# Performance work log

Hardware: AMD Instinct MI355X
Metric: run time of the kernel (lower is better)

## Reference

```python
import jax, jax.numpy as jnp
import numpy as np

E = 8          # num_experts
TOP_K = 2      # experts per token
D = 1024       # hidden_size
F = 2048       # intermediate_size
B, S = 2, 2048


def setup_inputs() -> dict:
    key = jax.random.key(0)
    k0, k1, k2, k3, k4 = jax.random.split(key, 5)
    return {
        "hidden_states": jax.random.normal(k0, (B, S, D), dtype=jnp.float32),
        "gate_w": jax.random.normal(k1, (D, E), dtype=jnp.float32) * 0.02,
        "w1": jax.random.normal(k2, (E, D, F), dtype=jnp.float32) * 0.02,
        "w2": jax.random.normal(k3, (E, F, D), dtype=jnp.float32) * 0.02,
        "w3": jax.random.normal(k4, (E, D, F), dtype=jnp.float32) * 0.02,
    }


def reference(hidden_states, gate_w, w1, w2, w3):
    b, s, d = hidden_states.shape
    x = hidden_states.reshape(-1, d)                       # [T, D]
    router_logits = x @ gate_w                             # [T, E]
    probs = jax.nn.softmax(router_logits, axis=-1)
    top_w, top_i = jax.lax.top_k(probs, TOP_K)             # [T, K]
    top_w = top_w / jnp.sum(top_w, axis=-1, keepdims=True)

    out = jnp.zeros_like(x)
    for e in range(E):
        # combine weight for expert e per token (0 if not routed here)
        w_e = jnp.sum(jnp.where(top_i == e, top_w, 0.0), axis=-1)   # [T]
        act = jax.nn.silu(x @ w1[e]) * (x @ w3[e])                  # [T, F]
        out = out + (act @ w2[e]) * w_e[:, None]
    return out.reshape(b, s, d)
```

## Files before the change

kernel.cpp:

```cpp
#include <hip/hip_runtime.h>

#define T_TOK 4096
#define D_DIM 1024
#define F_DIM 2048
#define E_NUM 8
#define MAX_TILES 136

typedef __attribute__((ext_vector_type(8))) short bf16x8;
typedef __attribute__((ext_vector_type(4))) float f32x4;

__device__ __forceinline__ unsigned short f2bf(float f) {
  unsigned u = __builtin_bit_cast(unsigned, f);
  unsigned r = 0x7FFFu + ((u >> 16) & 1u);
  return (unsigned short)((u + r) >> 16);
}

__device__ __forceinline__ void gload16(const unsigned short* g, unsigned short* l) {
  __builtin_amdgcn_global_load_lds(
      (const __attribute__((address_space(1))) unsigned int*)g,
      (__attribute__((address_space(3))) unsigned int*)l, 16, 0, 0);
}

__device__ __forceinline__ f32x4 mfma16(bf16x8 a, bf16x8 b, f32x4 c) {
  return __builtin_amdgcn_mfma_f32_16x16x32_bf16(a, b, c, 0, 0, 0);
}

__global__ __launch_bounds__(256) void transpose_all_kernel(
    const float* __restrict__ w1, const float* __restrict__ w3,
    const float* __restrict__ w2,
    unsigned short* __restrict__ W1t, unsigned short* __restrict__ W3t,
    unsigned short* __restrict__ W2t) {
  __shared__ float tile[64][65];
  int z = blockIdx.z;
  int which = z >> 3, e = z & 7;
  const float* src; unsigned short* dst; int M, N;
  if (which == 0)      { src = w1; dst = W1t; M = D_DIM; N = F_DIM; }
  else if (which == 1) { src = w3; dst = W3t; M = D_DIM; N = F_DIM; }
  else                 { src = w2; dst = W2t; M = F_DIM; N = D_DIM; }
  src += (size_t)e * M * N; dst += (size_t)e * M * N;
  int bid = blockIdx.y * gridDim.x + blockIdx.x;
  int nbx = N / 64;
  int i0 = (bid / nbx) * 64, j0 = (bid % nbx) * 64;
  int tid = threadIdx.x;
  int lr = tid >> 4;
  int lc = (tid & 15) * 4;
  #pragma unroll
  for (int p = 0; p < 4; p++) {
    int row = p * 16 + lr;
    float4 v = *(const float4*)&src[(size_t)(i0 + row) * N + j0 + lc];
    tile[row][lc + 0] = v.x; tile[row][lc + 1] = v.y;
    tile[row][lc + 2] = v.z; tile[row][lc + 3] = v.w;
  }
  __syncthreads();
  #pragma unroll
  for (int p = 0; p < 4; p++) {
    int orow = p * 16 + lr;
    unsigned short b0 = f2bf(tile[lc + 0][orow]);
    unsigned short b1 = f2bf(tile[lc + 1][orow]);
    unsigned short b2 = f2bf(tile[lc + 2][orow]);
    unsigned short b3 = f2bf(tile[lc + 3][orow]);
    uint2 o;
    o.x = b0 | ((unsigned)b1 << 16);
    o.y = b2 | ((unsigned)b3 << 16);
    *(uint2*)&dst[(size_t)(j0 + orow) * M + i0 + lc] = o;
  }
}

__global__ __launch_bounds__(256) void logits_kernel(const float* __restrict__ x,
                                                     const float* __restrict__ gw,
                                                     int* __restrict__ route_e,
                                                     float2* __restrict__ route_w,
                                                     unsigned short* __restrict__ Xb) {
  int lane = threadIdx.x & 63;
  int t = blockIdx.x * 4 + (threadIdx.x >> 6);
  float acc[E_NUM];
  #pragma unroll
  for (int e = 0; e < E_NUM; e++) acc[e] = 0.f;
  const float* xr = x + (size_t)t * D_DIM;
  unsigned short* xbr = Xb + (size_t)t * D_DIM;
  #pragma unroll
  for (int j = 0; j < D_DIM / 64; j++) {
    int d = lane + 64 * j;
    float xv = xr[d];
    xbr[d] = f2bf(xv);
    const float4* g = reinterpret_cast<const float4*>(gw + (size_t)d * E_NUM);
    float4 g0 = g[0], g1 = g[1];
    acc[0] += xv * g0.x; acc[1] += xv * g0.y; acc[2] += xv * g0.z; acc[3] += xv * g0.w;
    acc[4] += xv * g1.x; acc[5] += xv * g1.y; acc[6] += xv * g1.z; acc[7] += xv * g1.w;
  }
  #pragma unroll
  for (int e = 0; e < E_NUM; e++) {
    #pragma unroll
    for (int off = 32; off > 0; off >>= 1) acc[e] += __shfl_xor(acc[e], off);
  }
  if (lane == 0) {
    int e1 = 0; float l1 = acc[0];
    #pragma unroll
    for (int e = 1; e < E_NUM; e++) { if (acc[e] > l1) { l1 = acc[e]; e1 = e; } }
    int e2 = -1; float l2 = -1e30f;
    #pragma unroll
    for (int e = 0; e < E_NUM; e++) { if (e != e1 && acc[e] > l2) { l2 = acc[e]; e2 = e; } }
    float wa = 1.f / (1.f + expf(l2 - l1));
    float wb = 1.f / (1.f + expf(l1 - l2));
    route_e[t] = e1 | (e2 << 8);
    route_w[t] = make_float2(wa, wb);
  }
}

__global__ __launch_bounds__(1024) void scatter_kernel(
    const int* __restrict__ route_e, const float2* __restrict__ route_w,
    int* __restrict__ counts, int4* __restrict__ tiles,
    int* __restrict__ list, float* __restrict__ wts) {
  int tid = threadIdx.x;
  int lane = tid & 63, wv = tid >> 6;
  __shared__ int wave_tot[16][E_NUM];
  __shared__ int wave_base[16][E_NUM];
  __shared__ int tot_s[E_NUM];

  int e_loc[8]; float w_loc[8];
  #pragma unroll
  for (int j = 0; j < 4; j++) {
    int t = tid * 4 + j;
    int re = route_e[t];
    float2 rw = route_w[t];
    e_loc[2 * j]     = re & 0xff; w_loc[2 * j]     = rw.x;
    e_loc[2 * j + 1] = re >> 8;   w_loc[2 * j + 1] = rw.y;
  }
  int c[E_NUM], pre[E_NUM];
  #pragma unroll
  for (int e = 0; e < E_NUM; e++) {
    int s = 0;
    #pragma unroll
    for (int j = 0; j < 8; j++) s += (e_loc[j] == e) ? 1 : 0;
    c[e] = s;
  }
  #pragma unroll
  for (int e = 0; e < E_NUM; e++) {
    int v = c[e];
    #pragma unroll
    for (int off = 1; off < 64; off <<= 1) {
      int u = __shfl_up(v, off);
      if (lane >= off) v += u;
    }
    pre[e] = v - c[e];
    if (lane == 63) wave_tot[wv][e] = v;
  }
  __syncthreads();
  if (tid < E_NUM) {
    int s = 0;
    for (int w = 0; w < 16; w++) { wave_base[w][tid] = s; s += wave_tot[w][tid]; }
    tot_s[tid] = s;
    counts[tid] = s;
  }
  __syncthreads();
  #pragma unroll
  for (int j = 0; j < 8; j++) {
    int e = e_loc[j];
    int off = 0;
    #pragma unroll
    for (int jj = 0; jj < 8; jj++)
      if (jj < j) off += (e_loc[jj] == e) ? 1 : 0;
    int basee = 0, pree = 0;
    #pragma unroll
    for (int ee = 0; ee < E_NUM; ee++)
      if (e == ee) { basee = wave_base[wv][ee]; pree = pre[ee]; }
    int pos = basee + pree + off;
    int t = tid * 4 + (j >> 1);
    list[e * T_TOK + pos] = t * 2 + (j & 1);
    wts[e * T_TOK + pos]  = w_loc[j];
  }
  if (tid < MAX_TILES) {
    int4 tt; tt.x = -1; tt.y = 0; tt.z = 0; tt.w = 0;
    int s = 0;
    #pragma unroll
    for (int e = 0; e < E_NUM; e++) {
      int ntl = (tot_s[e] + 63) >> 6;
      if (tid >= s && tid < s + ntl) { tt.x = e; tt.y = (tid - s) * 64; tt.z = tot_s[e]; }
      s += ntl;
    }
    tiles[tid] = tt;
  }
}

__global__ __launch_bounds__(256, 4) void gemm1_kernel(
    const unsigned short* __restrict__ Xb,
    const unsigned short* __restrict__ W1t,
    const unsigned short* __restrict__ W3t,
    const int4* __restrict__ tiles, const int* __restrict__ list,
    unsigned short* __restrict__ H) {
  __shared__ unsigned short As[64 * 64];
  __shared__ unsigned short B1s[64 * 64];
  __shared__ unsigned short B3s[64 * 64];
  __shared__ int rid_s[64];

  int4 td = tiles[blockIdx.y];
  int e = td.x;
  if (e < 0) return;
  int base = td.y, cnt = td.z;
  int nt = blockIdx.x;
  int tid = threadIdx.x;

  if (tid < 64) {
    int r = base + tid; if (r > cnt - 1) r = cnt - 1;
    rid_s[tid] = list[e * T_TOK + r];
  }
  __syncthreads();

  int lane = tid & 63, wid = tid >> 6;
  int sr = lane >> 3;
  int sg = (lane & 7) ^ sr;
  const unsigned short* a_src[2];
  #pragma unroll
  for (int t = 0; t < 2; t++)
    a_src[t] = Xb + (size_t)(rid_s[wid * 16 + t * 8 + sr] >> 1) * D_DIM + sg * 8;
  const unsigned short *b1_src[2], *b3_src[2];
  #pragma unroll
  for (int t = 0; t < 2; t++) {
    size_t row = (size_t)e * F_DIM + nt * 64 + wid * 16 + t * 8 + sr;
    b1_src[t] = W1t + row * D_DIM + sg * 8;
    b3_src[t] = W3t + row * D_DIM + sg * 8;
  }

  int wm = (wid >> 1) * 32, wn = (wid & 1) * 32;
  int frow = lane & 15;
  int fk = lane >> 4;

  unsigned offA[2][2], offB[2][2];
  #pragma unroll
  for (int mf = 0; mf < 2; mf++)
    #pragma unroll
    for (int kc = 0; kc < 2; kc++) {
      int m = wm + mf * 16 + frow, gk = kc * 4 + fk;
      offA[mf][kc] = m * 64 + ((gk ^ (m & 7)) * 8);
    }
  #pragma unroll
  for (int nf = 0; nf < 2; nf++)
    #pragma unroll
    for (int kc = 0; kc < 2; kc++) {
      int n = wn + nf * 16 + frow, gk = kc * 4 + fk;
      offB[nf][kc] = n * 64 + ((gk ^ (n & 7)) * 8);
    }

  f32x4 acc1[2][2], acc3[2][2];
  #pragma unroll
  for (int mf = 0; mf < 2; mf++)
    #pragma unroll
    for (int nf = 0; nf < 2; nf++) {
      f32x4 z = {0.f, 0.f, 0.f, 0.f};
      acc1[mf][nf] = z; acc3[mf][nf] = z;
    }

  #pragma unroll 1
  for (int k0 = 0; k0 < D_DIM; k0 += 64) {
    #pragma unroll
    for (int t = 0; t < 2; t++) {
      gload16(a_src[t] + k0, &As[(wid * 16 + t * 8) * 64]);
      gload16(b1_src[t] + k0, &B1s[(wid * 16 + t * 8) * 64]);
      gload16(b3_src[t] + k0, &B3s[(wid * 16 + t * 8) * 64]);
    }
    __syncthreads();
    #pragma unroll
    for (int kc = 0; kc < 2; kc++) {
      bf16x8 a[2], b1[2], b3[2];
      #pragma unroll
      for (int mf = 0; mf < 2; mf++) a[mf] = *(const bf16x8*)&As[offA[mf][kc]];
      #pragma unroll
      for (int nf = 0; nf < 2; nf++) {
        b1[nf] = *(const bf16x8*)&B1s[offB[nf][kc]];
        b3[nf] = *(const bf16x8*)&B3s[offB[nf][kc]];
      }
      #pragma unroll
      for (int mf = 0; mf < 2; mf++)
        #pragma unroll
        for (int nf = 0; nf < 2; nf++) {
          acc1[mf][nf] = mfma16(a[mf], b1[nf], acc1[mf][nf]);
          acc3[mf][nf] = mfma16(a[mf], b3[nf], acc3[mf][nf]);
        }
    }
    __syncthreads();
  }

  #pragma unroll
  for (int mf = 0; mf < 2; mf++) {
    #pragma unroll
    for (int i = 0; i < 4; i++) {
      int m = wm + mf * 16 + fk * 4 + i;
      if (base + m < cnt) {
        int rid = rid_s[m];
        unsigned short* hrow = H + (size_t)rid * F_DIM + nt * 64 + wn;
        #pragma unroll
        for (int nf = 0; nf < 2; nf++) {
          float z = acc1[mf][nf][i];
          float u = acc3[mf][nf][i];
          hrow[nf * 16 + frow] = f2bf((z / (1.f + expf(-z))) * u);
        }
      }
    }
  }
}

__global__ __launch_bounds__(256, 4) void gemm2_kernel(
    const unsigned short* __restrict__ H,
    const unsigned short* __restrict__ W2t,
    const int4* __restrict__ tiles, const int* __restrict__ list,
    const float* __restrict__ wts,
    float* __restrict__ out) {
  __shared__ unsigned short As[64 * 64];
  __shared__ unsigned short Bs[128 * 64];
  __shared__ int rid_s[64];
  __shared__ float wt_s[64];

  int4 td = tiles[blockIdx.y];
  int e = td.x;
  if (e < 0) return;
  int base = td.y, cnt = td.z;
  int nt = blockIdx.x;
  int tid = threadIdx.x;

  if (tid < 64) {
    int r = base + tid; if (r > cnt - 1) r = cnt - 1;
    rid_s[tid] = list[e * T_TOK + r];
    wt_s[tid] = wts[e * T_TOK + r];
  }
  __syncthreads();

  int lane = tid & 63, wid = tid >> 6;
  int sr = lane >> 3;
  int sg = (lane & 7) ^ sr;
  const unsigned short* a_src[2];
  #pragma unroll
  for (int t = 0; t < 2; t++)
    a_src[t] = H + (size_t)rid_s[wid * 16 + t * 8 + sr] * F_DIM + sg * 8;
  const unsigned short* b_src[4];
  #pragma unroll
  for (int t = 0; t < 4; t++)
    b_src[t] = W2t + ((size_t)e * D_DIM + nt * 128 + wid * 32 + t * 8 + sr) * F_DIM + sg * 8;

  int wm = (wid >> 1) * 32, wn = (wid & 1) * 64;
  int frow = lane & 15;
  int fk = lane >> 4;

  unsigned offA[2][2], offB[4][2];
  #pragma unroll
  for (int mf = 0; mf < 2; mf++)
    #pragma unroll
    for (int kc = 0; kc < 2; kc++) {
      int m = wm + mf * 16 + frow, gk = kc * 4 + fk;
      offA[mf][kc] = m * 64 + ((gk ^ (m & 7)) * 8);
    }
  #pragma unroll
  for (int nf = 0; nf < 4; nf++)
    #pragma unroll
    for (int kc = 0; kc < 2; kc++) {
      int n = wn + nf * 16 + frow, gk = kc * 4 + fk;
      offB[nf][kc] = n * 64 + ((gk ^ (n & 7)) * 8);
    }

  f32x4 acc[2][4];
  #pragma unroll
  for (int mf = 0; mf < 2; mf++)
    #pragma unroll
    for (int nf = 0; nf < 4; nf++) {
      f32x4 z = {0.f, 0.f, 0.f, 0.f};
      acc[mf][nf] = z;
    }

  #pragma unroll 1
  for (int k0 = 0; k0 < F_DIM; k0 += 64) {
    #pragma unroll
    for (int t = 0; t < 2; t++)
      gload16(a_src[t] + k0, &As[(wid * 16 + t * 8) * 64]);
    #pragma unroll
    for (int t = 0; t < 4; t++)
      gload16(b_src[t] + k0, &Bs[(wid * 32 + t * 8) * 64]);
    __syncthreads();
    #pragma unroll
    for (int kc = 0; kc < 2; kc++) {
      bf16x8 a[2], b[4];
      #pragma unroll
      for (int mf = 0; mf < 2; mf++) a[mf] = *(const bf16x8*)&As[offA[mf][kc]];
      #pragma unroll
      for (int nf = 0; nf < 4; nf++) b[nf] = *(const bf16x8*)&Bs[offB[nf][kc]];
      #pragma unroll
      for (int mf = 0; mf < 2; mf++)
        #pragma unroll
        for (int nf = 0; nf < 4; nf++)
          acc[mf][nf] = mfma16(a[mf], b[nf], acc[mf][nf]);
    }
    __syncthreads();
  }

  #pragma unroll
  for (int mf = 0; mf < 2; mf++) {
    #pragma unroll
    for (int i = 0; i < 4; i++) {
      int m = wm + mf * 16 + fk * 4 + i;
      if (base + m < cnt) {
        int tok = rid_s[m] >> 1;
        float w = wt_s[m];
        float* orow = out + (size_t)tok * D_DIM + nt * 128 + wn;
        #pragma unroll
        for (int nf = 0; nf < 4; nf++)
          atomicAdd(&orow[nf * 16 + frow], acc[mf][nf][i] * w);
      }
    }
  }
}

extern "C" void kernel_launch(void* const* d_in, const int* in_sizes, int n_in,
                              void* d_out, int out_size, void* d_ws, size_t ws_size,
                              hipStream_t stream) {
  const float* x  = (const float*)d_in[0];
  const float* gw = (const float*)d_in[1];
  const float* w1 = (const float*)d_in[2];
  const float* w2 = (const float*)d_in[3];
  const float* w3 = (const float*)d_in[4];
  float* out = (float*)d_out;

  char* ws = (char*)d_ws;
  const size_t LISTB = (size_t)E_NUM * T_TOK * 4;
  size_t o_counts  = 0;
  size_t o_tiles   = 256;
  size_t o_route_e = 4096;
  size_t o_route_w = o_route_e + (size_t)T_TOK * 4;
  size_t o_list    = o_route_w + (size_t)T_TOK * 8;
  size_t o_wts     = o_list + LISTB;
  size_t o_Xb      = o_wts + LISTB;
  size_t o_W1t     = o_Xb + (size_t)T_TOK * D_DIM * 2;
  size_t wt_sz     = (size_t)E_NUM * F_DIM * D_DIM * 2;
  size_t o_W3t     = o_W1t + wt_sz;
  size_t o_W2t     = o_W3t + wt_sz;
  size_t o_H       = o_W2t + wt_sz;

  int* counts   = (int*)(ws + o_counts);
  int4* tiles   = (int4*)(ws + o_tiles);
  int* route_e  = (int*)(ws + o_route_e);
  float2* route_w = (float2*)(ws + o_route_w);
  int* list     = (int*)(ws + o_list);
  float* wts    = (float*)(ws + o_wts);
  unsigned short* Xb  = (unsigned short*)(ws + o_Xb);
  unsigned short* W1t = (unsigned short*)(ws + o_W1t);
  unsigned short* W3t = (unsigned short*)(ws + o_W3t);
  unsigned short* W2t = (unsigned short*)(ws + o_W2t);
  unsigned short* H   = (unsigned short*)(ws + o_H);

  hipMemsetAsync(out, 0, (size_t)out_size * 4, stream);

  transpose_all_kernel<<<dim3(32, 16, 24), 256, 0, stream>>>(
      w1, w3, w2, W1t, W3t, W2t);

  logits_kernel<<<dim3(T_TOK / 4), 256, 0, stream>>>(x, gw, route_e, route_w, Xb);
  scatter_kernel<<<dim3(1), 1024, 0, stream>>>(route_e, route_w, counts, tiles, list, wts);

  gemm1_kernel<<<dim3(F_DIM / 64, MAX_TILES), 256, 0, stream>>>(
      Xb, W1t, W3t, tiles, list, H);
  gemm2_kernel<<<dim3(D_DIM / 128, MAX_TILES), 256, 0, stream>>>(
      H, W2t, tiles, list, wts, out);
}
```

Measured before the change: 241.1 us.

## Double-buffer LDS loads and enlarge token tiles to 128 rows in MoE GEMMs

Doubles the token tile height from 64 to 128 rows in both expert GEMMs, so each wave computes 64x32 (gemm1) or 64x64 (gemm2) outputs and more work is reused per weight load. It also adds LDS double buffering with explicit vmcnt waits and barriers, so the next K-slice is loaded while the current one is computed. The aim is to hide global-load latency and cut weight-tile reloads. The cost is more LDS and registers per block, which lowers occupancy, and more padded rows in each expert's last tile.

```diff
diff --git a/kernel.cpp b/kernel.cpp
--- a/kernel.cpp
+++ b/kernel.cpp
@@ -4,7 +4,7 @@
 #define D_DIM 1024
 #define F_DIM 2048
 #define E_NUM 8
-#define MAX_TILES 136
+#define MAX_TILES 72
 
 typedef __attribute__((ext_vector_type(8))) short bf16x8;
 typedef __attribute__((ext_vector_type(4))) float f32x4;
@@ -24,6 +24,9 @@
 __device__ __forceinline__ f32x4 mfma16(bf16x8 a, bf16x8 b, f32x4 c) {
   return __builtin_amdgcn_mfma_f32_16x16x32_bf16(a, b, c, 0, 0, 0);
 }
+
+#define VMCNT(N) asm volatile("s_waitcnt vmcnt(" #N ")" ::: "memory")
+#define BAR() __builtin_amdgcn_s_barrier()
 
 __global__ __launch_bounds__(256) void transpose_all_kernel(
     const float* __restrict__ w1, const float* __restrict__ w3,
@@ -174,24 +177,24 @@
     int s = 0;
     #pragma unroll
     for (int e = 0; e < E_NUM; e++) {
-      int ntl = (tot_s[e] + 63) >> 6;
-      if (tid >= s && tid < s + ntl) { tt.x = e; tt.y = (tid - s) * 64; tt.z = tot_s[e]; }
+      int ntl = (tot_s[e] + 127) >> 7;
+      if (tid >= s && tid < s + ntl) { tt.x = e; tt.y = (tid - s) * 128; tt.z = tot_s[e]; }
       s += ntl;
     }
     tiles[tid] = tt;
   }
 }
 
-__global__ __launch_bounds__(256, 4) void gemm1_kernel(
+__global__ __launch_bounds__(256) void gemm1_kernel(
     const unsigned short* __restrict__ Xb,
     const unsigned short* __restrict__ W1t,
     const unsigned short* __restrict__ W3t,
     const int4* __restrict__ tiles, const int* __restrict__ list,
     unsigned short* __restrict__ H) {
-  __shared__ unsigned short As[64 * 64];
-  __shared__ unsigned short B1s[64 * 64];
-  __shared__ unsigned short B3s[64 * 64];
-  __shared__ int rid_s[64];
+  __shared__ unsigned short As[2][128 * 64];
+  __shared__ unsigned short B1s[2][64 * 64];
+  __shared__ unsigned short B3s[2][64 * 64];
+  __shared__ int rid_s[128];
 
   int4 td = tiles[blockIdx.y];
   int e = td.x;
@@ -200,7 +203,7 @@
   int nt = blockIdx.x;
   int tid = threadIdx.x;
 
-  if (tid < 64) {
+  if (tid < 128) {
     int r = base + tid; if (r > cnt - 1) r = cnt - 1;
     rid_s[tid] = list[e * T_TOK + r];
   }
@@ -209,10 +212,10 @@
   int lane = tid & 63, wid = tid >> 6;
   int sr = lane >> 3;
   int sg = (lane & 7) ^ sr;
-  const unsigned short* a_src[2];
-  #pragma unroll
-  for (int t = 0; t < 2; t++)
-    a_src[t] = Xb + (size_t)(rid_s[wid * 16 + t * 8 + sr] >> 1) * D_DIM + sg * 8;
+  const unsigned short* a_src[4];
+  #pragma unroll
+  for (int t = 0; t < 4; t++)
+    a_src[t] = Xb + (size_t)(rid_s[wid * 32 + t * 8 + sr] >> 1) * D_DIM + sg * 8;
   const unsigned short *b1_src[2], *b3_src[2];
   #pragma unroll
   for (int t = 0; t < 2; t++) {
@@ -221,13 +224,13 @@
     b3_src[t] = W3t + row * D_DIM + sg * 8;
   }
 
-  int wm = (wid >> 1) * 32, wn = (wid & 1) * 32;
+  int wm = (wid >> 1) * 64, wn = (wid & 1) * 32;
   int frow = lane & 15;
   int fk = lane >> 4;
 
-  unsigned offA[2][2], offB[2][2];
-  #pragma unroll
-  for (int mf = 0; mf < 2; mf++)
+  unsigned offA[4][2], offB[2][2];
+  #pragma unroll
+  for (int mf = 0; mf < 4; mf++)
     #pragma unroll
     for (int kc = 0; kc < 2; kc++) {
       int m = wm + mf * 16 + frow, gk = kc * 4 + fk;
@@ -241,47 +244,63 @@
       offB[nf][kc] = n * 64 + ((gk ^ (n & 7)) * 8);
     }
 
-  f32x4 acc1[2][2], acc3[2][2];
-  #pragma unroll
-  for (int mf = 0; mf < 2; mf++)
+  f32x4 acc1[4][2], acc3[4][2];
+  #pragma unroll
+  for (int mf = 0; mf < 4; mf++)
     #pragma unroll
     for (int nf = 0; nf < 2; nf++) {
       f32x4 z = {0.f, 0.f, 0.f, 0.f};
       acc1[mf][nf] = z; acc3[mf][nf] = z;
     }
 
-  #pragma unroll 1
-  for (int k0 = 0; k0 < D_DIM; k0 += 64) {
+  auto stage = [&](int b, int k0) {
+    #pragma unroll
+    for (int t = 0; t < 4; t++)
+      gload16(a_src[t] + k0, &As[b][(wid * 32 + t * 8) * 64]);
     #pragma unroll
     for (int t = 0; t < 2; t++) {
-      gload16(a_src[t] + k0, &As[(wid * 16 + t * 8) * 64]);
-      gload16(b1_src[t] + k0, &B1s[(wid * 16 + t * 8) * 64]);
-      gload16(b3_src[t] + k0, &B3s[(wid * 16 + t * 8) * 64]);
-    }
-    __syncthreads();
-    #pragma unroll
-    for (int kc = 0; kc < 2; kc++) {
-      bf16x8 a[2], b1[2], b3[2];
-      #pragma unroll
-      for (int mf = 0; mf < 2; mf++) a[mf] = *(const bf16x8*)&As[offA[mf][kc]];
+      gload16(b1_src[t] + k0, &B1s[b][(wid * 16 + t * 8) * 64]);
+      gload16(b3_src[t] + k0, &B3s[b][(wid * 16 + t * 8) * 64]);
+    }
+  };
+  auto compute = [&](int b) {
+    #pragma unroll
+    for (int kc = 0; kc < 2; kc++) {
+      bf16x8 a[4], b1[2], b3[2];
+      #pragma unroll
+      for (int mf = 0; mf < 4; mf++) a[mf] = *(const bf16x8*)&As[b][offA[mf][kc]];
       #pragma unroll
       for (int nf = 0; nf < 2; nf++) {
-        b1[nf] = *(const bf16x8*)&B1s[offB[nf][kc]];
-        b3[nf] = *(const bf16x8*)&B3s[offB[nf][kc]];
+        b1[nf] = *(const bf16x8*)&B1s[b][offB[nf][kc]];
+        b3[nf] = *(const bf16x8*)&B3s[b][offB[nf][kc]];
       }
       #pragma unroll
-      for (int mf = 0; mf < 2; mf++)
+      for (int mf = 0; mf < 4; mf++)
         #pragma unroll
         for (int nf = 0; nf < 2; nf++) {
           acc1[mf][nf] = mfma16(a[mf], b1[nf], acc1[mf][nf]);
           acc3[mf][nf] = mfma16(a[mf], b3[nf], acc3[mf][nf]);
         }
     }
-    __syncthreads();
-  }
-
-  #pragma unroll
-  for (int mf = 0; mf < 2; mf++) {
+  };
+
+  stage(0, 0);
+  int cur = 0;
+  #pragma unroll 1
+  for (int k0 = 64; k0 < D_DIM; k0 += 64) {
+    stage(cur ^ 1, k0);
+    VMCNT(8);
+    BAR();
+    compute(cur);
+    BAR();
+    cur ^= 1;
+  }
+  VMCNT(0);
+  BAR();
+  compute(cur);
+
+  #pragma unroll
+  for (int mf = 0; mf < 4; mf++) {
     #pragma unroll
     for (int i = 0; i < 4; i++) {
       int m = wm + mf * 16 + fk * 4 + i;
@@ -299,16 +318,16 @@
   }
 }
 
-__global__ __launch_bounds__(256, 4) void gemm2_kernel(
+__global__ __launch_bounds__(256) void gemm2_kernel(
     const unsigned short* __restrict__ H,
     const unsigned short* __restrict__ W2t,
     const int4* __restrict__ tiles, const int* __restrict__ list,
     const float* __restrict__ wts,
     float* __restrict__ out) {
-  __shared__ unsigned short As[64 * 64];
-  __shared__ unsigned short Bs[128 * 64];
-  __shared__ int rid_s[64];
-  __shared__ float wt_s[64];
+  __shared__ unsigned short As[2][128 * 64];
+  __shared__ unsigned short Bs[2][128 * 64];
+  __shared__ int rid_s[128];
+  __shared__ float wt_s[128];
 
   int4 td = tiles[blockIdx.y];
   int e = td.x;
@@ -317,7 +336,7 @@
   int nt = blockIdx.x;
   int tid = threadIdx.x;
 
-  if (tid < 64) {
+  if (tid < 128) {
     int r = base + tid; if (r > cnt - 1) r = cnt - 1;
     rid_s[tid] = list[e * T_TOK + r];
     wt_s[tid] = wts[e * T_TOK + r];
@@ -327,22 +346,22 @@
   int lane = tid & 63, wid = tid >> 6;
   int sr = lane >> 3;
   int sg = (lane & 7) ^ sr;
-  const unsigned short* a_src[2];
-  #pragma unroll
-  for (int t = 0; t < 2; t++)
-    a_src[t] = H + (size_t)rid_s[wid * 16 + t * 8 + sr] * F_DIM + sg * 8;
+  const unsigned short* a_src[4];
+  #pragma unroll
+  for (int t = 0; t < 4; t++)
+    a_src[t] = H + (size_t)rid_s[wid * 32 + t * 8 + sr] * F_DIM + sg * 8;
   const unsigned short* b_src[4];
   #pragma unroll
   for (int t = 0; t < 4; t++)
     b_src[t] = W2t + ((size_t)e * D_DIM + nt * 128 + wid * 32 + t * 8 + sr) * F_DIM + sg * 8;
 
-  int wm = (wid >> 1) * 32, wn = (wid & 1) * 64;
+  int wm = (wid >> 1) * 64, wn = (wid & 1) * 64;
   int frow = lane & 15;
   int fk = lane >> 4;
 
-  unsigned offA[2][2], offB[4][2];
-  #pragma unroll
-  for (int mf = 0; mf < 2; mf++)
+  unsigned offA[4][2], offB[4][2];
+  #pragma unroll
+  for (int mf = 0; mf < 4; mf++)
     #pragma unroll
     for (int kc = 0; kc < 2; kc++) {
       int m = wm + mf * 16 + frow, gk = kc * 4 + fk;
@@ -356,42 +375,55 @@
       offB[nf][kc] = n * 64 + ((gk ^ (n & 7)) * 8);
     }
 
-  f32x4 acc[2][4];
-  #pragma unroll
-  for (int mf = 0; mf < 2; mf++)
+  f32x4 acc[4][4];
+  #pragma unroll
+  for (int mf = 0; mf < 4; mf++)
     #pragma unroll
     for (int nf = 0; nf < 4; nf++) {
       f32x4 z = {0.f, 0.f, 0.f, 0.f};
       acc[mf][nf] = z;
     }
 
-  #pragma unroll 1
-  for (int k0 = 0; k0 < F_DIM; k0 += 64) {
-    #pragma unroll
-    for (int t = 0; t < 2; t++)
-      gload16(a_src[t] + k0, &As[(wid * 16 + t * 8) * 64]);
-    #pragma unroll
-    for (int t = 0; t < 4; t++)
-      gload16(b_src[t] + k0, &Bs[(wid * 32 + t * 8) * 64]);
-    __syncthreads();
-    #pragma unroll
-    for (int kc = 0; kc < 2; kc++) {
-      bf16x8 a[2], b[4];
-      #pragma unroll
-      for (int mf = 0; mf < 2; mf++) a[mf] = *(const bf16x8*)&As[offA[mf][kc]];
-      #pragma unroll
-      for (int nf = 0; nf < 4; nf++) b[nf] = *(const bf16x8*)&Bs[offB[nf][kc]];
-      #pragma unroll
-      for (int mf = 0; mf < 2; mf++)
+  auto stage = [&](int b, int k0) {
+    #pragma unroll
+    for (int t = 0; t < 4; t++) {
+      gload16(a_src[t] + k0, &As[b][(wid * 32 + t * 8) * 64]);
+      gload16(b_src[t] + k0, &Bs[b][(wid * 32 + t * 8) * 64]);
+    }
+  };
+  auto compute = [&](int bb) {
+    #pragma unroll
+    for (int kc = 0; kc < 2; kc++) {
+      bf16x8 a[4], b[4];
+      #pragma unroll
+      for (int mf = 0; mf < 4; mf++) a[mf] = *(const bf16x8*)&As[bb][offA[mf][kc]];
+      #pragma unroll
+      for (int nf = 0; nf < 4; nf++) b[nf] = *(const bf16x8*)&Bs[bb][offB[nf][kc]];
+      #pragma unroll
+      for (int mf = 0; mf < 4; mf++)
         #pragma unroll
         for (int nf = 0; nf < 4; nf++)
           acc[mf][nf] = mfma16(a[mf], b[nf], acc[mf][nf]);
     }
-    __syncthreads();
-  }
-
-  #pragma unroll
-  for (int mf = 0; mf < 2; mf++) {
+  };
+
+  stage(0, 0);
+  int cur = 0;
+  #pragma unroll 1
+  for (int k0 = 64; k0 < F_DIM; k0 += 64) {
+    stage(cur ^ 1, k0);
+    VMCNT(8);
+    BAR();
+    compute(cur);
+    BAR();
+    cur ^= 1;
+  }
+  VMCNT(0);
+  BAR();
+  compute(cur);
+
+  #pragma unroll
+  for (int mf = 0; mf < 4; mf++) {
     #pragma unroll
     for (int i = 0; i < 4; i++) {
       int m = wm + mf * 16 + fk * 4 + i;
```

Result: slower. 282.7 us (+17.2%).

## Enlarge gemm1 to 256x128 tiles with double-buffered LDS pipeline

Applied to the files above, without the earlier changes.

The gate/up GEMM now uses 256-token by 128-column tiles with 512 threads and a dynamic 128 KB LDS double buffer. Global-to-LDS loads for the next k-tile are issued while MFMAs run on the current one, with s_setprio around the MFMA blocks. The scatter kernel now emits a second tile table at 256-token granularity for this kernel. The aim is more reuse of weights and activations per block and hiding load latency, at the cost of lower occupancy and more padding waste on partial tiles.

```diff
diff --git a/kernel.cpp b/kernel.cpp
--- a/kernel.cpp
+++ b/kernel.cpp
@@ -4,18 +4,20 @@
 #define D_DIM 1024
 #define F_DIM 2048
 #define E_NUM 8
-#define MAX_TILES 136
+#define T64 136
+#define T256 48
 
 typedef __attribute__((ext_vector_type(8))) short bf16x8;
 typedef __attribute__((ext_vector_type(4))) float f32x4;
-
-__device__ __forceinline__ unsigned short f2bf(float f) {
+typedef unsigned short us;
+
+__device__ __forceinline__ us f2bf(float f) {
   unsigned u = __builtin_bit_cast(unsigned, f);
   unsigned r = 0x7FFFu + ((u >> 16) & 1u);
-  return (unsigned short)((u + r) >> 16);
-}
-
-__device__ __forceinline__ void gload16(const unsigned short* g, unsigned short* l) {
+  return (us)((u + r) >> 16);
+}
+
+__device__ __forceinline__ void gload16(const us* g, us* l) {
   __builtin_amdgcn_global_load_lds(
       (const __attribute__((address_space(1))) unsigned int*)g,
       (__attribute__((address_space(3))) unsigned int*)l, 16, 0, 0);
@@ -25,15 +27,18 @@
   return __builtin_amdgcn_mfma_f32_16x16x32_bf16(a, b, c, 0, 0, 0);
 }
 
+#define VMCNT0() asm volatile("s_waitcnt vmcnt(0)" ::: "memory")
+#define BAR() __builtin_amdgcn_s_barrier()
+#define PRIO(x) __builtin_amdgcn_s_setprio(x)
+
 __global__ __launch_bounds__(256) void transpose_all_kernel(
     const float* __restrict__ w1, const float* __restrict__ w3,
     const float* __restrict__ w2,
-    unsigned short* __restrict__ W1t, unsigned short* __restrict__ W3t,
-    unsigned short* __restrict__ W2t) {
+    us* __restrict__ W1t, us* __restrict__ W3t, us* __restrict__ W2t) {
   __shared__ float tile[64][65];
   int z = blockIdx.z;
   int which = z >> 3, e = z & 7;
-  const float* src; unsigned short* dst; int M, N;
+  const float* src; us* dst; int M, N;
   if (which == 0)      { src = w1; dst = W1t; M = D_DIM; N = F_DIM; }
   else if (which == 1) { src = w3; dst = W3t; M = D_DIM; N = F_DIM; }
   else                 { src = w2; dst = W2t; M = F_DIM; N = D_DIM; }
@@ -42,8 +47,7 @@
   int nbx = N / 64;
   int i0 = (bid / nbx) * 64, j0 = (bid % nbx) * 64;
   int tid = threadIdx.x;
-  int lr = tid >> 4;
-  int lc = (tid & 15) * 4;
+  int lr = tid >> 4, lc = (tid & 15) * 4;
   #pragma unroll
   for (int p = 0; p < 4; p++) {
     int row = p * 16 + lr;
@@ -55,10 +59,10 @@
   #pragma unroll
   for (int p = 0; p < 4; p++) {
     int orow = p * 16 + lr;
-    unsigned short b0 = f2bf(tile[lc + 0][orow]);
-    unsigned short b1 = f2bf(tile[lc + 1][orow]);
-    unsigned short b2 = f2bf(tile[lc + 2][orow]);
-    unsigned short b3 = f2bf(tile[lc + 3][orow]);
+    us b0 = f2bf(tile[lc + 0][orow]);
+    us b1 = f2bf(tile[lc + 1][orow]);
+    us b2 = f2bf(tile[lc + 2][orow]);
+    us b3 = f2bf(tile[lc + 3][orow]);
     uint2 o;
     o.x = b0 | ((unsigned)b1 << 16);
     o.y = b2 | ((unsigned)b3 << 16);
@@ -70,14 +74,14 @@
                                                      const float* __restrict__ gw,
                                                      int* __restrict__ route_e,
                                                      float2* __restrict__ route_w,
-                                                     unsigned short* __restrict__ Xb) {
+                                                     us* __restrict__ Xb) {
   int lane = threadIdx.x & 63;
   int t = blockIdx.x * 4 + (threadIdx.x >> 6);
   float acc[E_NUM];
   #pragma unroll
   for (int e = 0; e < E_NUM; e++) acc[e] = 0.f;
   const float* xr = x + (size_t)t * D_DIM;
-  unsigned short* xbr = Xb + (size_t)t * D_DIM;
+  us* xbr = Xb + (size_t)t * D_DIM;
   #pragma unroll
   for (int j = 0; j < D_DIM / 64; j++) {
     int d = lane + 64 * j;
@@ -109,7 +113,7 @@
 
 __global__ __launch_bounds__(1024) void scatter_kernel(
     const int* __restrict__ route_e, const float2* __restrict__ route_w,
-    int* __restrict__ counts, int4* __restrict__ tiles,
+    int* __restrict__ counts, int4* __restrict__ tiles64, int4* __restrict__ tiles256,
     int* __restrict__ list, float* __restrict__ wts) {
   int tid = threadIdx.x;
   int lane = tid & 63, wv = tid >> 6;
@@ -169,7 +173,7 @@
     list[e * T_TOK + pos] = t * 2 + (j & 1);
     wts[e * T_TOK + pos]  = w_loc[j];
   }
-  if (tid < MAX_TILES) {
+  if (tid < T64) {
     int4 tt; tt.x = -1; tt.y = 0; tt.z = 0; tt.w = 0;
     int s = 0;
     #pragma unroll
@@ -178,20 +182,29 @@
       if (tid >= s && tid < s + ntl) { tt.x = e; tt.y = (tid - s) * 64; tt.z = tot_s[e]; }
       s += ntl;
     }
-    tiles[tid] = tt;
-  }
-}
-
-__global__ __launch_bounds__(256, 4) void gemm1_kernel(
-    const unsigned short* __restrict__ Xb,
-    const unsigned short* __restrict__ W1t,
-    const unsigned short* __restrict__ W3t,
+    tiles64[tid] = tt;
+  }
+  if (tid < T256) {
+    int4 tt; tt.x = -1; tt.y = 0; tt.z = 0; tt.w = 0;
+    int s = 0;
+    #pragma unroll
+    for (int e = 0; e < E_NUM; e++) {
+      int ntl = (tot_s[e] + 255) >> 8;
+      if (tid >= s && tid < s + ntl) { tt.x = e; tt.y = (tid - s) * 256; tt.z = tot_s[e]; }
+      s += ntl;
+    }
+    tiles256[tid] = tt;
+  }
+}
+
+__global__ __launch_bounds__(512, 2) void gemm1_kernel(
+    const us* __restrict__ Xb,
+    const us* __restrict__ W1t,
+    const us* __restrict__ W3t,
     const int4* __restrict__ tiles, const int* __restrict__ list,
-    unsigned short* __restrict__ H) {
-  __shared__ unsigned short As[64 * 64];
-  __shared__ unsigned short B1s[64 * 64];
-  __shared__ unsigned short B3s[64 * 64];
-  __shared__ int rid_s[64];
+    us* __restrict__ H) {
+  extern __shared__ us smem[];
+  __shared__ int rid_s[256];
 
   int4 td = tiles[blockIdx.y];
   int e = td.x;
@@ -200,7 +213,7 @@
   int nt = blockIdx.x;
   int tid = threadIdx.x;
 
-  if (tid < 64) {
+  if (tid < 256) {
     int r = base + tid; if (r > cnt - 1) r = cnt - 1;
     rid_s[tid] = list[e * T_TOK + r];
   }
@@ -209,87 +222,137 @@
   int lane = tid & 63, wid = tid >> 6;
   int sr = lane >> 3;
   int sg = (lane & 7) ^ sr;
-  const unsigned short* a_src[2];
-  #pragma unroll
-  for (int t = 0; t < 2; t++)
-    a_src[t] = Xb + (size_t)(rid_s[wid * 16 + t * 8 + sr] >> 1) * D_DIM + sg * 8;
-  const unsigned short *b1_src[2], *b3_src[2];
+  const us* a_src[4];
+  #pragma unroll
+  for (int t = 0; t < 4; t++)
+    a_src[t] = Xb + (size_t)(rid_s[wid * 32 + t * 8 + sr] >> 1) * D_DIM + sg * 8;
+  const us *b1_src[2], *b3_src[2];
   #pragma unroll
   for (int t = 0; t < 2; t++) {
-    size_t row = (size_t)e * F_DIM + nt * 64 + wid * 16 + t * 8 + sr;
+    size_t row = (size_t)e * F_DIM + nt * 128 + wid * 16 + t * 8 + sr;
     b1_src[t] = W1t + row * D_DIM + sg * 8;
     b3_src[t] = W3t + row * D_DIM + sg * 8;
   }
 
-  int wm = (wid >> 1) * 32, wn = (wid & 1) * 32;
+  int wm = (wid >> 1) * 64, wn = (wid & 1) * 64;
   int frow = lane & 15;
   int fk = lane >> 4;
 
-  unsigned offA[2][2], offB[2][2];
-  #pragma unroll
-  for (int mf = 0; mf < 2; mf++)
+  unsigned offA[4][2], offB[4][2];
+  #pragma unroll
+  for (int mf = 0; mf < 4; mf++)
     #pragma unroll
     for (int kc = 0; kc < 2; kc++) {
       int m = wm + mf * 16 + frow, gk = kc * 4 + fk;
       offA[mf][kc] = m * 64 + ((gk ^ (m & 7)) * 8);
     }
   #pragma unroll
-  for (int nf = 0; nf < 2; nf++)
+  for (int nf = 0; nf < 4; nf++)
     #pragma unroll
     for (int kc = 0; kc < 2; kc++) {
       int n = wn + nf * 16 + frow, gk = kc * 4 + fk;
       offB[nf][kc] = n * 64 + ((gk ^ (n & 7)) * 8);
     }
 
-  f32x4 acc1[2][2], acc3[2][2];
-  #pragma unroll
-  for (int mf = 0; mf < 2; mf++)
-    #pragma unroll
-    for (int nf = 0; nf < 2; nf++) {
+  f32x4 acc1[4][4], acc3[4][4];
+  #pragma unroll
+  for (int mf = 0; mf < 4; mf++)
+    #pragma unroll
+    for (int nf = 0; nf < 4; nf++) {
       f32x4 z = {0.f, 0.f, 0.f, 0.f};
       acc1[mf][nf] = z; acc3[mf][nf] = z;
     }
 
+  us* A0 = smem;              us* A1 = smem + 32768;
+  us* B10 = A0 + 16384;       us* B11 = A1 + 16384;
+  us* B30 = B10 + 8192;       us* B31 = B11 + 8192;
+  int ldsA = (wid * 32) * 64;
+  int ldsB = (wid * 16) * 64;
+
+  auto stageA = [&](us* An, int k0) {
+    #pragma unroll
+    for (int t = 0; t < 4; t++) gload16(a_src[t] + k0, An + ldsA + t * 512);
+  };
+  auto stageB = [&](us* B1n, us* B3n, int k0) {
+    #pragma unroll
+    for (int t = 0; t < 2; t++) {
+      gload16(b1_src[t] + k0, B1n + ldsB + t * 512);
+      gload16(b3_src[t] + k0, B3n + ldsB + t * 512);
+    }
+  };
+
+  auto ktile = [&](const us* Ac, const us* B1c, const us* B3c,
+                   us* An, us* B1n, us* B3n, int k_next, bool more) {
+    bf16x8 a0[4], a1[4], bf[4];
+    if (more) stageA(An, k_next);
+    #pragma unroll
+    for (int mf = 0; mf < 4; mf++) a0[mf] = *(const bf16x8*)&Ac[offA[mf][0]];
+    #pragma unroll
+    for (int nf = 0; nf < 4; nf++) bf[nf] = *(const bf16x8*)&B1c[offB[nf][0]];
+    PRIO(1);
+    #pragma unroll
+    for (int mf = 0; mf < 4; mf++)
+      #pragma unroll
+      for (int nf = 0; nf < 4; nf++)
+        acc1[mf][nf] = mfma16(a0[mf], bf[nf], acc1[mf][nf]);
+    PRIO(0);
+    BAR();
+    if (more) stageB(B1n, B3n, k_next);
+    #pragma unroll
+    for (int nf = 0; nf < 4; nf++) bf[nf] = *(const bf16x8*)&B3c[offB[nf][0]];
+    PRIO(1);
+    #pragma unroll
+    for (int mf = 0; mf < 4; mf++)
+      #pragma unroll
+      for (int nf = 0; nf < 4; nf++)
+        acc3[mf][nf] = mfma16(a0[mf], bf[nf], acc3[mf][nf]);
+    PRIO(0);
+    BAR();
+    #pragma unroll
+    for (int mf = 0; mf < 4; mf++) a1[mf] = *(const bf16x8*)&Ac[offA[mf][1]];
+    #pragma unroll
+    for (int nf = 0; nf < 4; nf++) bf[nf] = *(const bf16x8*)&B1c[offB[nf][1]];
+    PRIO(1);
+    #pragma unroll
+    for (int mf = 0; mf < 4; mf++)
+      #pragma unroll
+      for (int nf = 0; nf < 4; nf++)
+        acc1[mf][nf] = mfma16(a1[mf], bf[nf], acc1[mf][nf]);
+    PRIO(0);
+    BAR();
+    #pragma unroll
+    for (int nf = 0; nf < 4; nf++) bf[nf] = *(const bf16x8*)&B3c[offB[nf][1]];
+    PRIO(1);
+    #pragma unroll
+    for (int mf = 0; mf < 4; mf++)
+      #pragma unroll
+      for (int nf = 0; nf < 4; nf++)
+        acc3[mf][nf] = mfma16(a1[mf], bf[nf], acc3[mf][nf]);
+    PRIO(0);
+    if (more) VMCNT0();
+    BAR();
+  };
+
+  stageA(A0, 0);
+  stageB(B10, B30, 0);
+  VMCNT0();
+  BAR();
   #pragma unroll 1
-  for (int k0 = 0; k0 < D_DIM; k0 += 64) {
-    #pragma unroll
-    for (int t = 0; t < 2; t++) {
-      gload16(a_src[t] + k0, &As[(wid * 16 + t * 8) * 64]);
-      gload16(b1_src[t] + k0, &B1s[(wid * 16 + t * 8) * 64]);
-      gload16(b3_src[t] + k0, &B3s[(wid * 16 + t * 8) * 64]);
-    }
-    __syncthreads();
-    #pragma unroll
-    for (int kc = 0; kc < 2; kc++) {
-      bf16x8 a[2], b1[2], b3[2];
-      #pragma unroll
-      for (int mf = 0; mf < 2; mf++) a[mf] = *(const bf16x8*)&As[offA[mf][kc]];
-      #pragma unroll
-      for (int nf = 0; nf < 2; nf++) {
-        b1[nf] = *(const bf16x8*)&B1s[offB[nf][kc]];
-        b3[nf] = *(const bf16x8*)&B3s[offB[nf][kc]];
-      }
-      #pragma unroll
-      for (int mf = 0; mf < 2; mf++)
-        #pragma unroll
-        for (int nf = 0; nf < 2; nf++) {
-          acc1[mf][nf] = mfma16(a[mf], b1[nf], acc1[mf][nf]);
-          acc3[mf][nf] = mfma16(a[mf], b3[nf], acc3[mf][nf]);
-        }
-    }
-    __syncthreads();
-  }
-
-  #pragma unroll
-  for (int mf = 0; mf < 2; mf++) {
+  for (int kt = 0; kt < 16; kt += 2) {
+    ktile(A0, B10, B30, A1, B11, B31, (kt + 1) * 64, true);
+    ktile(A1, B11, B31, A0, B10, B30, (kt + 2) * 64, kt + 2 < 16);
+  }
+
+  #pragma unroll
+  for (int mf = 0; mf < 4; mf++) {
     #pragma unroll
     for (int i = 0; i < 4; i++) {
       int m = wm + mf * 16 + fk * 4 + i;
       if (base + m < cnt) {
         int rid = rid_s[m];
-        unsigned short* hrow = H + (size_t)rid * F_DIM + nt * 64 + wn;
+        us* hrow = H + (size_t)rid * F_DIM + nt * 128 + wn;
         #pragma unroll
-        for (int nf = 0; nf < 2; nf++) {
+        for (int nf = 0; nf < 4; nf++) {
           float z = acc1[mf][nf][i];
           float u = acc3[mf][nf][i];
           hrow[nf * 16 + frow] = f2bf((z / (1.f + expf(-z))) * u);
@@ -300,13 +363,13 @@
 }
 
 __global__ __launch_bounds__(256, 4) void gemm2_kernel(
-    const unsigned short* __restrict__ H,
-    const unsigned short* __restrict__ W2t,
+    const us* __restrict__ H,
+    const us* __restrict__ W2t,
     const int4* __restrict__ tiles, const int* __restrict__ list,
     const float* __restrict__ wts,
     float* __restrict__ out) {
-  __shared__ unsigned short As[64 * 64];
-  __shared__ unsigned short Bs[128 * 64];
+  __shared__ us As[64 * 64];
+  __shared__ us Bs[128 * 64];
   __shared__ int rid_s[64];
   __shared__ float wt_s[64];
 
@@ -327,11 +390,11 @@
   int lane = tid & 63, wid = tid >> 6;
   int sr = lane >> 3;
   int sg = (lane & 7) ^ sr;
-  const unsigned short* a_src[2];
+  const us* a_src[2];
   #pragma unroll
   for (int t = 0; t < 2; t++)
     a_src[t] = H + (size_t)rid_s[wid * 16 + t * 8 + sr] * F_DIM + sg * 8;
-  const unsigned short* b_src[4];
+  const us* b_src[4];
   #pragma unroll
   for (int t = 0; t < 4; t++)
     b_src[t] = W2t + ((size_t)e * D_DIM + nt * 128 + wid * 32 + t * 8 + sr) * F_DIM + sg * 8;
@@ -420,7 +483,8 @@
   char* ws = (char*)d_ws;
   const size_t LISTB = (size_t)E_NUM * T_TOK * 4;
   size_t o_counts  = 0;
-  size_t o_tiles   = 256;
+  size_t o_t64     = 256;
+  size_t o_t256    = 2560;
   size_t o_route_e = 4096;
   size_t o_route_w = o_route_e + (size_t)T_TOK * 4;
   size_t o_list    = o_route_w + (size_t)T_TOK * 8;
@@ -432,17 +496,21 @@
   size_t o_W2t     = o_W3t + wt_sz;
   size_t o_H       = o_W2t + wt_sz;
 
-  int* counts   = (int*)(ws + o_counts);
-  int4* tiles   = (int4*)(ws + o_tiles);
-  int* route_e  = (int*)(ws + o_route_e);
+  int* counts    = (int*)(ws + o_counts);
+  int4* tiles64  = (int4*)(ws + o_t64);
+  int4* tiles256 = (int4*)(ws + o_t256);
+  int* route_e   = (int*)(ws + o_route_e);
   float2* route_w = (float2*)(ws + o_route_w);
-  int* list     = (int*)(ws + o_list);
-  float* wts    = (float*)(ws + o_wts);
-  unsigned short* Xb  = (unsigned short*)(ws + o_Xb);
-  unsigned short* W1t = (unsigned short*)(ws + o_W1t);
-  unsigned short* W3t = (unsigned short*)(ws + o_W3t);
-  unsigned short* W2t = (unsigned short*)(ws + o_W2t);
-  unsigned short* H   = (unsigned short*)(ws + o_H);
+  int* list      = (int*)(ws + o_list);
+  float* wts     = (float*)(ws + o_wts);
+  us* Xb  = (us*)(ws + o_Xb);
+  us* W1t = (us*)(ws + o_W1t);
+  us* W3t = (us*)(ws + o_W3t);
+  us* W2t = (us*)(ws + o_W2t);
+  us* H   = (us*)(ws + o_H);
+
+  hipFuncSetAttribute((const void*)gemm1_kernel,
+                      hipFuncAttributeMaxDynamicSharedMemorySize, 131072);
 
   hipMemsetAsync(out, 0, (size_t)out_size * 4, stream);
 
@@ -450,10 +518,11 @@
       w1, w3, w2, W1t, W3t, W2t);
 
   logits_kernel<<<dim3(T_TOK / 4), 256, 0, stream>>>(x, gw, route_e, route_w, Xb);
-  scatter_kernel<<<dim3(1), 1024, 0, stream>>>(route_e, route_w, counts, tiles, list, wts);
-
-  gemm1_kernel<<<dim3(F_DIM / 64, MAX_TILES), 256, 0, stream>>>(
-      Xb, W1t, W3t, tiles, list, H);
-  gemm2_kernel<<<dim3(D_DIM / 128, MAX_TILES), 256, 0, stream>>>(
-      H, W2t, tiles, list, wts, out);
-}
+  scatter_kernel<<<dim3(1), 1024, 0, stream>>>(route_e, route_w, counts,
+                                               tiles64, tiles256, list, wts);
+
+  gemm1_kernel<<<dim3(F_DIM / 128, T256), 512, 131072, stream>>>(
+      Xb, W1t, W3t, tiles256, list, H);
+  gemm2_kernel<<<dim3(D_DIM / 128, T64), 256, 0, stream>>>(
+      H, W2t, tiles64, list, wts, out);
+}
```

Result: slower. 297.2 us (+23.2%).
